# Performance work log

Measured on AMD Instinct MI355X. Metric: run time of the kernel, lower is better.

## Reference

```python
import jax, jax.numpy as jnp
import numpy as np

N, E = 15000, 60000
IN_FEATS, EMB_N, EMB_E, HID = 32, 16, 16, 64
NODE_DIM = IN_FEATS + 2 * EMB_N          # 64
EDGE_DIM = 2 * EMB_E + 1                 # 33
N_SUPER, N_NT, N_TAG, N_PRI = 16, 32, 64, 128


def setup_inputs() -> dict:
    key = jax.random.key(0)
    ks = jax.random.split(key, 24)
    s = lambda d: 1.0 / np.sqrt(d)
    inp = {
        'x': jax.random.normal(ks[0], (N, IN_FEATS), jnp.float32),
        'input_np': jax.random.randint(ks[1], (N,), 0, 1000, jnp.int32),
        'output_np': jax.random.randint(ks[2], (N,), 0, 1000, jnp.int32),
        'edge_index': jax.random.randint(ks[3], (2, E), 0, N, jnp.int32),
        'edge_nt': jax.random.randint(ks[4], (E,), 0, 50, jnp.int32),
        'edge_np': jax.random.randint(ks[5], (E,), 0, 500, jnp.int32),
        'edge_sc': jax.random.uniform(ks[6], (E,), jnp.float32),
        # embeddings
        'in_np_emb': jax.random.normal(ks[7], (1000, EMB_N), jnp.float32),
        'out_np_emb': jax.random.normal(ks[8], (1000, EMB_N), jnp.float32),
        'edge_np_emb': jax.random.normal(ks[9], (500, EMB_E), jnp.float32),
        'edge_nt_emb': jax.random.normal(ks[10], (50, EMB_E), jnp.float32),
        # edge MLP: Linear(33,64) -> ReLU -> Linear(64, NODE_DIM*HID)
        'mlp_w1': jax.random.normal(ks[11], (EDGE_DIM, 64), jnp.float32) * s(EDGE_DIM),
        'mlp_b1': jnp.zeros((64,), jnp.float32),
        'mlp_w2': jax.random.normal(ks[12], (64, NODE_DIM * HID), jnp.float32) * s(64),
        'mlp_b2': jnp.zeros((NODE_DIM * HID,), jnp.float32),
        # NNConv root weight + bias
        'root_w': jax.random.normal(ks[13], (NODE_DIM, HID), jnp.float32) * s(NODE_DIM),
        'conv_b': jnp.zeros((HID,), jnp.float32),
        # heads
        'w_super': jax.random.normal(ks[14], (HID, N_SUPER), jnp.float32) * s(HID),
        'b_super': jnp.zeros((N_SUPER,), jnp.float32),
        'w_nt': jax.random.normal(ks[15], (HID, N_NT), jnp.float32) * s(HID),
        'b_nt': jnp.zeros((N_NT,), jnp.float32),
        'w_tags': jax.random.normal(ks[16], (HID, N_TAG), jnp.float32) * s(HID),
        'b_tags': jnp.zeros((N_TAG,), jnp.float32),
        'w_primary': jax.random.normal(ks[17], (HID, N_PRI), jnp.float32) * s(HID),
        'b_primary': jnp.zeros((N_PRI,), jnp.float32),
    }
    return inp


def _forward(x, edge_sc, in_np_emb, out_np_emb, edge_np_emb, edge_nt_emb,
             mlp_w1, mlp_b1, mlp_w2, mlp_b2, root_w, conv_b,
             w_super, b_super, w_nt, b_nt, w_tags, b_tags, w_primary, b_primary,
             input_np, output_np, edge_index, edge_nt, edge_np):
    # node features: [N, NODE_DIM]
    xf = jnp.concatenate([x, in_np_emb[input_np], out_np_emb[output_np]], axis=1)
    # edge features: [E, EDGE_DIM]
    ea = jnp.concatenate([edge_nt_emb[edge_nt], edge_np_emb[edge_np], edge_sc[:, None]], axis=1)
    # edge MLP -> per-edge weight matrix [E, NODE_DIM, HID]
    h = jax.nn.relu(ea @ mlp_w1 + mlp_b1)
    W = (h @ mlp_w2 + mlp_b2).reshape(-1, NODE_DIM, HID)
    src, dst = edge_index[0], edge_index[1]
    # per-edge matvec: message from src node through its edge weight
    msg = jnp.einsum('ei,eio->eo', xf[src], W)                     # [E, HID]
    sums = jax.ops.segment_sum(msg, dst, num_segments=N)            # [N, HID]
    cnt = jax.ops.segment_sum(jnp.ones((msg.shape[0],), msg.dtype), dst, num_segments=N)
    aggr = sums / jnp.maximum(cnt, 1.0)[:, None]                    # scatter-mean
    out = jax.nn.relu(aggr + xf @ root_w + conv_b)                  # NNConv root + bias, then ReLU
    # dropout is identity in eval mode
    return (out @ w_super + b_super, out @ w_nt + b_nt,
            out @ w_tags + b_tags, out @ w_primary + b_primary)


def reference(x, input_np, output_np, edge_index, edge_nt, edge_np, edge_sc,
              in_np_emb, out_np_emb, edge_np_emb, edge_nt_emb,
              mlp_w1, mlp_b1, mlp_w2, mlp_b2, root_w, conv_b,
              w_super, b_super, w_nt, b_nt, w_tags, b_tags, w_primary, b_primary):
    return _forward(x, edge_sc, in_np_emb, out_np_emb, edge_np_emb, edge_nt_emb,
                    mlp_w1, mlp_b1, mlp_w2, mlp_b2, root_w, conv_b,
                    w_super, b_super, w_nt, b_nt, w_tags, b_tags, w_primary, b_primary,
                    input_np, output_np, edge_index, edge_nt, edge_np)
```

## Files before the change

kernel.cpp:

```cpp
#include <hip/hip_runtime.h>
#include <stdint.h>

#define NN 15000
#define NE 60000

typedef unsigned short u16;
typedef __attribute__((ext_vector_type(8))) short short8;
typedef __attribute__((ext_vector_type(4))) float f32x4;

#define XF_OFF    0u
#define W2T_OFF   1920000u
#define ROOTT_OFF 2452480u
#define WCATT_OFF 2460672u
#define SUMS_OFF  2491392u
#define H2_OFF    6391392u

__device__ __forceinline__ unsigned cvtpk(float lo, float hi) {
    unsigned r;
    asm("v_cvt_pk_bf16_f32 %0, %1, %2" : "=v"(r) : "v"(lo), "v"(hi));
    return r;
}
__device__ __forceinline__ u16 f2b(float f) { return (u16)(cvtpk(f, f) & 0xffffu); }

__global__ __launch_bounds__(256) void k_pre(
        const float* __restrict__ x,
        const int* __restrict__ inp, const int* __restrict__ outp,
        const int* __restrict__ ent, const int* __restrict__ enp,
        const float* __restrict__ esc,
        const float* __restrict__ in_emb, const float* __restrict__ out_emb,
        const float* __restrict__ nt_emb, const float* __restrict__ np_emb,
        const float* __restrict__ w1, const float* __restrict__ b1,
        const float* __restrict__ w2, const float* __restrict__ b2,
        const float* __restrict__ rootw,
        const float* __restrict__ wsup, const float* __restrict__ wnt,
        const float* __restrict__ wtg, const float* __restrict__ wpr,
        u16* __restrict__ xf, u16* __restrict__ w2t,
        u16* __restrict__ rootT, u16* __restrict__ wcatT,
        u16* __restrict__ h2, float4* __restrict__ zbase) {
    const int bid = blockIdx.x, tid = threadIdx.x;
    if (bid < 469) {
        __shared__ float w1f[33 * 64];
        __shared__ float b1f[64];
        __shared__ float ea[128][34];
        const int e0 = bid * 128;
        for (int i = tid; i < 33 * 64; i += 256) w1f[i] = w1[i];
        if (tid < 64) b1f[tid] = b1[tid];
        for (int idx = tid; idx < 128 * 33; idx += 256) {
            int le = idx / 33, f = idx - le * 33;
            int e = e0 + le;
            float v = 0.f;
            if (e < NE) {
                if (f < 16)      v = nt_emb[ent[e] * 16 + f];
                else if (f < 32) v = np_emb[enp[e] * 16 + (f - 16)];
                else             v = esc[e];
            }
            ea[le][f] = v;
        }
        __syncthreads();
        const int c = tid & 63, eg = tid >> 6;
        unsigned pk[16];
        #pragma unroll
        for (int l = 0; l < 32; l += 2) {
            float a0 = b1f[c], a1 = b1f[c];
            #pragma unroll
            for (int i = 0; i < 33; ++i) {
                a0 += ea[eg * 32 + l][i] * w1f[i * 64 + c];
                a1 += ea[eg * 32 + l + 1][i] * w1f[i * 64 + c];
            }
            pk[l >> 1] = cvtpk(fmaxf(a0, 0.f), fmaxf(a1, 0.f));
        }
        const int ew = e0 + eg * 32;
        if (ew + 32 <= NE) {
            #pragma unroll
            for (int g = 0; g < 8; ++g)
                *(uint2*)(h2 + (size_t)((ew >> 2) + g) * 256 + c * 4) =
                    make_uint2(pk[2 * g], pk[2 * g + 1]);
        }
    } else if (bid < 1407) {
        int t = (bid - 469) * 256 + tid;
        if (t >= NN * 16) return;
        int n = t >> 4, j4 = t & 15;
        float4 v;
        if (j4 < 8)       v = *(const float4*)(x + n * 32 + j4 * 4);
        else if (j4 < 12) v = *(const float4*)(in_emb + inp[n] * 16 + (j4 - 8) * 4);
        else              v = *(const float4*)(out_emb + outp[n] * 16 + (j4 - 12) * 4);
        uint2 p;
        p.x = cvtpk(v.x, v.y);
        p.y = cvtpk(v.z, v.w);
        *(uint2*)(xf + n * 64 + j4 * 4) = p;
    } else if (bid < 2523) {
        int idx = (bid - 1407) * 256 + tid;
        if (idx < 65 * 4096) {
            int k = idx >> 12, r = idx & 4095, o = r >> 6, i = r & 63;
            float v = (k < 64) ? w2[(k << 12) + (i << 6) + o] : b2[(i << 6) + o];
            w2t[idx] = f2b(v);
        } else if (idx < 65 * 4096 + 4096) {
            int t = idx - 65 * 4096; int c = t >> 6, i = t & 63;
            rootT[t] = f2b(rootw[i * 64 + c]);
        } else if (idx < 65 * 4096 + 4096 + 15360) {
            int t = idx - (65 * 4096 + 4096); int col = t >> 6, k = t & 63;
            float v;
            if (col < 16)       v = wsup[k * 16 + col];
            else if (col < 48)  v = wnt[k * 32 + col - 16];
            else if (col < 112) v = wtg[k * 64 + col - 48];
            else                v = wpr[k * 128 + col - 112];
            wcatT[t] = f2b(v);
        }
    } else {
        int i = (bid - 2523) * 256 + tid;
        if (i < (NN * 65) / 4) zbase[i] = make_float4(0.f, 0.f, 0.f, 0.f);
    }
}

__global__ __launch_bounds__(1024) void k_msg(const int* __restrict__ ei,
                                              const u16* __restrict__ xf,
                                              const u16* __restrict__ h2,
                                              const u16* __restrict__ w2t,
                                              float* __restrict__ sums,
                                              float* __restrict__ cnt) {
    __shared__ __align__(16) char smem[65 * 2048];
    const int tid  = threadIdx.x;
    const int lane = tid & 63;
    const int wave = tid >> 6;
    const int lhi  = lane >> 4;
    const int llo  = lane & 15;
    const int oq   = blockIdx.x & 3;
    const int wslot = (blockIdx.x >> 2) * 16 + wave;

    for (int sl = wave; sl < 65; sl += 16) {
        const char* src = (const char*)w2t + (size_t)sl * 8192 + oq * 2048;
        char* dst = smem + sl * 2048;
        #pragma unroll
        for (int it = 0; it < 2; ++it) {
            int lin = (lane + it * 64) * 16;
            int phys = lin ^ (((lin >> 7) & 7) << 4);
            *(uint4*)(dst + phys) = *(const uint4*)(src + lin);
        }
    }
    __syncthreads();
    if (wslot >= 938) return;

    const int pc0 = (llo * 128 + lhi * 16) ^ ((llo & 7) << 4);
    const int pc1 = (llo * 128 + 64 + lhi * 16) ^ ((llo & 7) << 4);

    const int base = wslot * 64;
    short8 a[4][2]; int eb[4];
    #pragma unroll
    for (int st = 0; st < 4; ++st) {
        int e = base + st * 16 + llo;
        int src = ei[e < NE ? e : NE - 1];
        a[st][0] = *(const short8*)(xf + (size_t)src * 64 + lhi * 8);
        a[st][1] = *(const short8*)(xf + (size_t)src * 64 + 32 + lhi * 8);
        int e2 = base + st * 16 + lhi * 4;
        eb[st] = (e2 > NE - 4) ? (NE - 4) : e2;
    }
    f32x4 acc[4];
    #pragma unroll
    for (int st = 0; st < 4; ++st) acc[st] = (f32x4){0.f, 0.f, 0.f, 0.f};

    uint4 hc[4], hn[4];
    #pragma unroll
    for (int st = 0; st < 4; ++st)
        hc[st] = *(const uint4*)(h2 + ((size_t)(eb[st] >> 2) << 8));

    #pragma unroll 1
    for (int s = 0; s < 64; s += 2) {
        if (s + 2 < 64) {
            #pragma unroll
            for (int st = 0; st < 4; ++st)
                hn[st] = *(const uint4*)(h2 + ((size_t)(eb[st] >> 2) << 8) + (s + 2) * 4);
        }
        {
            const char* bb = smem + s * 2048;
            short8 B0 = *(const short8*)(bb + pc0);
            short8 B1 = *(const short8*)(bb + pc1);
            #pragma unroll
            for (int st = 0; st < 4; ++st) {
                f32x4 q;
                q = __builtin_amdgcn_mfma_f32_16x16x32_bf16(a[st][0], B0, (f32x4){0.f,0.f,0.f,0.f}, 0, 0, 0);
                q = __builtin_amdgcn_mfma_f32_16x16x32_bf16(a[st][1], B1, q, 0, 0, 0);
                union { unsigned u; float f; } u0, u1, u2, u3;
                u0.u = hc[st].x << 16;         u1.u = hc[st].x & 0xffff0000u;
                u2.u = hc[st].y << 16;         u3.u = hc[st].y & 0xffff0000u;
                acc[st][0] = fmaf(u0.f, q[0], acc[st][0]);
                acc[st][1] = fmaf(u1.f, q[1], acc[st][1]);
                acc[st][2] = fmaf(u2.f, q[2], acc[st][2]);
                acc[st][3] = fmaf(u3.f, q[3], acc[st][3]);
            }
        }
        {
            const char* bb = smem + (s + 1) * 2048;
            short8 B0 = *(const short8*)(bb + pc0);
            short8 B1 = *(const short8*)(bb + pc1);
            #pragma unroll
            for (int st = 0; st < 4; ++st) {
                f32x4 q;
                q = __builtin_amdgcn_mfma_f32_16x16x32_bf16(a[st][0], B0, (f32x4){0.f,0.f,0.f,0.f}, 0, 0, 0);
                q = __builtin_amdgcn_mfma_f32_16x16x32_bf16(a[st][1], B1, q, 0, 0, 0);
                union { unsigned u; float f; } u0, u1, u2, u3;
                u0.u = hc[st].z << 16;         u1.u = hc[st].z & 0xffff0000u;
                u2.u = hc[st].w << 16;         u3.u = hc[st].w & 0xffff0000u;
                acc[st][0] = fmaf(u0.f, q[0], acc[st][0]);
                acc[st][1] = fmaf(u1.f, q[1], acc[st][1]);
                acc[st][2] = fmaf(u2.f, q[2], acc[st][2]);
                acc[st][3] = fmaf(u3.f, q[3], acc[st][3]);
            }
        }
        #pragma unroll
        for (int st = 0; st < 4; ++st) hc[st] = hn[st];
    }
    {
        const char* bb = smem + 64 * 2048;
        short8 B0 = *(const short8*)(bb + pc0);
        short8 B1 = *(const short8*)(bb + pc1);
        #pragma unroll
        for (int st = 0; st < 4; ++st) {
            acc[st] = __builtin_amdgcn_mfma_f32_16x16x32_bf16(a[st][0], B0, acc[st], 0, 0, 0);
            acc[st] = __builtin_amdgcn_mfma_f32_16x16x32_bf16(a[st][1], B1, acc[st], 0, 0, 0);
        }
    }
    #pragma unroll
    for (int st = 0; st < 4; ++st) {
        int4 d4 = *(const int4*)(ei + NE + eb[st]);
        #pragma unroll
        for (int r = 0; r < 4; ++r) {
            int e = base + st * 16 + lhi * 4 + r;
            if (e < NE) {
                int d = (r == 0) ? d4.x : (r == 1) ? d4.y : (r == 2) ? d4.z : d4.w;
                atomicAdd(sums + (size_t)d * 64 + oq * 16 + llo, acc[st][r]);
                if (oq == 0 && llo == 0) atomicAdd(cnt + d, 1.0f);
            }
        }
    }
}

__global__ __launch_bounds__(256) void k_out(const u16* __restrict__ xf,
                                             const float* __restrict__ sums,
                                             const float* __restrict__ cnt,
                                             const u16* __restrict__ rootT,
                                             const u16* __restrict__ wcatT,
                                             const float* __restrict__ convb,
                                             const float* __restrict__ bsup,
                                             const float* __restrict__ bnt,
                                             const float* __restrict__ btg,
                                             const float* __restrict__ bpr,
                                             float* __restrict__ outp) {
    __shared__ __align__(16) u16 outlds[4][16][72];
    int tid = threadIdx.x;
    int wave = tid >> 6, lane = tid & 63;
    int lhi = lane >> 4, llo = lane & 15;
    int sid = blockIdx.x * 4 + wave;
    const bool live = (sid < 938);
    if (!live) sid = 937;
    int n0 = sid * 16;

    short8 a1[2];
    #pragma unroll
    for (int c = 0; c < 2; ++c) {
        int node = n0 + llo; if (node >= NN) node = NN - 1;
        a1[c] = *(const short8*)(xf + (size_t)node * 64 + c * 32 + lhi * 8);
    }
    f32x4 racc[4];
    #pragma unroll
    for (int o = 0; o < 4; ++o) racc[o] = (f32x4){0.f, 0.f, 0.f, 0.f};
    #pragma unroll
    for (int c = 0; c < 2; ++c)
        #pragma unroll
        for (int o = 0; o < 4; ++o) {
            short8 b = *(const short8*)(rootT + (o * 16 + llo) * 64 + c * 32 + lhi * 8);
            racc[o] = __builtin_amdgcn_mfma_f32_16x16x32_bf16(a1[c], b, racc[o], 0, 0, 0);
        }
    #pragma unroll
    for (int o = 0; o < 4; ++o) {
        int col = o * 16 + llo;
        #pragma unroll
        for (int r = 0; r < 4; ++r) {
            int node = n0 + lhi * 4 + r;
            float v = 0.f;
            if (node < NN) v = sums[(size_t)node * 64 + col] / fmaxf(cnt[node], 1.0f);
            v += racc[o][r] + convb[col];
            v = fmaxf(v, 0.f);
            outlds[wave][lhi * 4 + r][col] = f2b(v);
        }
    }
    __syncthreads();
    short8 a2[2];
    #pragma unroll
    for (int c = 0; c < 2; ++c)
        a2[c] = *(const short8*)(&outlds[wave][llo][c * 32 + lhi * 8]);
    #pragma unroll
    for (int o = 0; o < 15; ++o) {
        f32x4 hacc = (f32x4){0.f, 0.f, 0.f, 0.f};
        #pragma unroll
        for (int c = 0; c < 2; ++c) {
            short8 b = *(const short8*)(wcatT + (o * 16 + llo) * 64 + c * 32 + lhi * 8);
            hacc = __builtin_amdgcn_mfma_f32_16x16x32_bf16(a2[c], b, hacc, 0, 0, 0);
        }
        int col = o * 16 + llo;
        float bv; size_t off0; int w_, csh;
        if (col < 16)       { bv = bsup[col];       off0 = 0;                 w_ = 16;  csh = 0;   }
        else if (col < 48)  { bv = bnt[col - 16];   off0 = (size_t)NN * 16;   w_ = 32;  csh = 16;  }
        else if (col < 112) { bv = btg[col - 48];   off0 = (size_t)NN * 48;   w_ = 64;  csh = 48;  }
        else                { bv = bpr[col - 112];  off0 = (size_t)NN * 112;  w_ = 128; csh = 112; }
        #pragma unroll
        for (int r = 0; r < 4; ++r) {
            int node = n0 + lhi * 4 + r;
            if (live && node < NN)
                outp[off0 + (size_t)node * w_ + (col - csh)] = hacc[r] + bv;
        }
    }
}

extern "C" void kernel_launch(void* const* d_in, const int* in_sizes, int n_in,
                              void* d_out, int out_size, void* d_ws, size_t ws_size,
                              hipStream_t stream) {
    const float* x        = (const float*)d_in[0];
    const int* input_np   = (const int*)d_in[1];
    const int* output_np  = (const int*)d_in[2];
    const int* edge_idx   = (const int*)d_in[3];
    const int* edge_nt    = (const int*)d_in[4];
    const int* edge_np    = (const int*)d_in[5];
    const float* edge_sc  = (const float*)d_in[6];
    const float* in_emb   = (const float*)d_in[7];
    const float* out_emb  = (const float*)d_in[8];
    const float* enp_emb  = (const float*)d_in[9];
    const float* ent_emb  = (const float*)d_in[10];
    const float* w1       = (const float*)d_in[11];
    const float* b1       = (const float*)d_in[12];
    const float* w2       = (const float*)d_in[13];
    const float* b2       = (const float*)d_in[14];
    const float* rootw    = (const float*)d_in[15];
    const float* convb    = (const float*)d_in[16];
    const float* wsup     = (const float*)d_in[17];
    const float* bsup     = (const float*)d_in[18];
    const float* wnt      = (const float*)d_in[19];
    const float* bnt      = (const float*)d_in[20];
    const float* wtg      = (const float*)d_in[21];
    const float* btg      = (const float*)d_in[22];
    const float* wpr      = (const float*)d_in[23];
    const float* bpr      = (const float*)d_in[24];

    char* ws = (char*)d_ws;
    u16* xf    = (u16*)(ws + XF_OFF);
    u16* w2t   = (u16*)(ws + W2T_OFF);
    u16* rootT = (u16*)(ws + ROOTT_OFF);
    u16* wcatT = (u16*)(ws + WCATT_OFF);
    float* sums = (float*)(ws + SUMS_OFF);
    float* cnt  = sums + (size_t)NN * 64;
    u16* h2    = (u16*)(ws + H2_OFF);

    k_pre<<<3476, 256, 0, stream>>>(x, input_np, output_np, edge_nt, edge_np, edge_sc,
                                    in_emb, out_emb, ent_emb, enp_emb, w1, b1, w2, b2,
                                    rootw, wsup, wnt, wtg, wpr,
                                    xf, w2t, rootT, wcatT, h2, (float4*)sums);
    k_msg<<<236, 1024, 0, stream>>>(edge_idx, xf, h2, w2t, sums, cnt);
    k_out<<<235, 256, 0, stream>>>(xf, sums, cnt, rootT, wcatT, convb, bsup, bnt, btg, bpr, (float*)d_out);
}
```

Before: 94.35 us.

## Compute edge MLP first layer with bf16 MFMA and enlarge message grid

The first edge-MLP layer (33->64 with ReLU) in the pre-kernel moves from scalar FP32 FMAs over a shared-memory tile to bf16 MFMA 16x16x32 instructions. Each wave handles 16 edges, with the gathered embeddings converted to bf16 fragments and w1 transposed into LDS. This cuts the ALU cost of the stage but lowers input precision to bf16 before the first matmul. The message kernel's grid also grows from 236 to 256 blocks with a launch-bounds occupancy hint, presumably to cover all edges or fill all CUs.

```diff
diff --git a/kernel.cpp b/kernel.cpp
--- a/kernel.cpp
+++ b/kernel.cpp
@@ -38,46 +38,52 @@
         u16* __restrict__ rootT, u16* __restrict__ wcatT,
         u16* __restrict__ h2, float4* __restrict__ zbase) {
     const int bid = blockIdx.x, tid = threadIdx.x;
-    if (bid < 469) {
-        __shared__ float w1f[33 * 64];
-        __shared__ float b1f[64];
-        __shared__ float ea[128][34];
-        const int e0 = bid * 128;
-        for (int i = tid; i < 33 * 64; i += 256) w1f[i] = w1[i];
-        if (tid < 64) b1f[tid] = b1[tid];
-        for (int idx = tid; idx < 128 * 33; idx += 256) {
-            int le = idx / 33, f = idx - le * 33;
-            int e = e0 + le;
-            float v = 0.f;
-            if (e < NE) {
-                if (f < 16)      v = nt_emb[ent[e] * 16 + f];
-                else if (f < 32) v = np_emb[enp[e] * 16 + (f - 16)];
-                else             v = esc[e];
-            }
-            ea[le][f] = v;
-        }
+    if (bid < 938) {
+        __shared__ __align__(16) u16 w1t[64 * 64];
+        __shared__ float b1s[64];
+        const int lane = tid & 63, wave = tid >> 6;
+        const int lhi = lane >> 4, llo = lane & 15;
+        for (int idx = tid; idx < 4096; idx += 256) {
+            int col = idx >> 6, k = idx & 63;
+            w1t[col * 64 + k] = f2b((k < 33) ? w1[k * 64 + col] : 0.f);
+        }
+        if (tid < 64) b1s[tid] = b1[tid];
         __syncthreads();
-        const int c = tid & 63, eg = tid >> 6;
-        unsigned pk[16];
-        #pragma unroll
-        for (int l = 0; l < 32; l += 2) {
-            float a0 = b1f[c], a1 = b1f[c];
-            #pragma unroll
-            for (int i = 0; i < 33; ++i) {
-                a0 += ea[eg * 32 + l][i] * w1f[i * 64 + c];
-                a1 += ea[eg * 32 + l + 1][i] * w1f[i * 64 + c];
-            }
-            pk[l >> 1] = cvtpk(fmaxf(a0, 0.f), fmaxf(a1, 0.f));
-        }
-        const int ew = e0 + eg * 32;
-        if (ew + 32 <= NE) {
-            #pragma unroll
-            for (int g = 0; g < 8; ++g)
-                *(uint2*)(h2 + (size_t)((ew >> 2) + g) * 256 + c * 4) =
-                    make_uint2(pk[2 * g], pk[2 * g + 1]);
-        }
-    } else if (bid < 1407) {
-        int t = (bid - 469) * 256 + tid;
+        int g = bid * 4 + wave;
+        if (g >= 3750) return;
+        int e = g * 16 + llo;
+        short8 A0;
+        {
+            const float* src = (lhi < 2) ? (nt_emb + (size_t)ent[e] * 16 + lhi * 8)
+                                         : (np_emb + (size_t)enp[e] * 16 + (lhi - 2) * 8);
+            float4 v0 = *(const float4*)(src);
+            float4 v1 = *(const float4*)(src + 4);
+            union { short8 s; unsigned u[4]; } Au;
+            Au.u[0] = cvtpk(v0.x, v0.y); Au.u[1] = cvtpk(v0.z, v0.w);
+            Au.u[2] = cvtpk(v1.x, v1.y); Au.u[3] = cvtpk(v1.z, v1.w);
+            A0 = Au.s;
+        }
+        short8 A1 = (short8){0, 0, 0, 0, 0, 0, 0, 0};
+        if (lhi == 0) {
+            union { short8 s; unsigned u[4]; } Au;
+            Au.s = A1; Au.u[0] = cvtpk(esc[e], 0.f); A1 = Au.s;
+        }
+        #pragma unroll
+        for (int o = 0; o < 4; ++o) {
+            short8 B0 = *(const short8*)(&w1t[(o * 16 + llo) * 64 + lhi * 8]);
+            short8 B1 = *(const short8*)(&w1t[(o * 16 + llo) * 64 + 32 + lhi * 8]);
+            f32x4 q;
+            q = __builtin_amdgcn_mfma_f32_16x16x32_bf16(A0, B0, (f32x4){0.f,0.f,0.f,0.f}, 0, 0, 0);
+            q = __builtin_amdgcn_mfma_f32_16x16x32_bf16(A1, B1, q, 0, 0, 0);
+            int kh = o * 16 + llo;
+            float bv = b1s[kh];
+            float v0 = fmaxf(q[0] + bv, 0.f), v1 = fmaxf(q[1] + bv, 0.f);
+            float v2 = fmaxf(q[2] + bv, 0.f), v3 = fmaxf(q[3] + bv, 0.f);
+            uint2 pk2 = make_uint2(cvtpk(v0, v1), cvtpk(v2, v3));
+            *(uint2*)(h2 + (size_t)(g * 4 + lhi) * 256 + kh * 4) = pk2;
+        }
+    } else if (bid < 1876) {
+        int t = (bid - 938) * 256 + tid;
         if (t >= NN * 16) return;
         int n = t >> 4, j4 = t & 15;
         float4 v;
@@ -88,8 +94,8 @@
         p.x = cvtpk(v.x, v.y);
         p.y = cvtpk(v.z, v.w);
         *(uint2*)(xf + n * 64 + j4 * 4) = p;
-    } else if (bid < 2523) {
-        int idx = (bid - 1407) * 256 + tid;
+    } else if (bid < 2992) {
+        int idx = (bid - 1876) * 256 + tid;
         if (idx < 65 * 4096) {
             int k = idx >> 12, r = idx & 4095, o = r >> 6, i = r & 63;
             float v = (k < 64) ? w2[(k << 12) + (i << 6) + o] : b2[(i << 6) + o];
@@ -107,17 +113,17 @@
             wcatT[t] = f2b(v);
         }
     } else {
-        int i = (bid - 2523) * 256 + tid;
+        int i = (bid - 2992) * 256 + tid;
         if (i < (NN * 65) / 4) zbase[i] = make_float4(0.f, 0.f, 0.f, 0.f);
     }
 }
 
-__global__ __launch_bounds__(1024) void k_msg(const int* __restrict__ ei,
-                                              const u16* __restrict__ xf,
-                                              const u16* __restrict__ h2,
-                                              const u16* __restrict__ w2t,
-                                              float* __restrict__ sums,
-                                              float* __restrict__ cnt) {
+__global__ __launch_bounds__(1024, 1) void k_msg(const int* __restrict__ ei,
+                                                 const u16* __restrict__ xf,
+                                                 const u16* __restrict__ h2,
+                                                 const u16* __restrict__ w2t,
+                                                 float* __restrict__ sums,
+                                                 float* __restrict__ cnt) {
     __shared__ __align__(16) char smem[65 * 2048];
     const int tid  = threadIdx.x;
     const int lane = tid & 63;
@@ -349,10 +355,10 @@
     float* cnt  = sums + (size_t)NN * 64;
     u16* h2    = (u16*)(ws + H2_OFF);
 
-    k_pre<<<3476, 256, 0, stream>>>(x, input_np, output_np, edge_nt, edge_np, edge_sc,
+    k_pre<<<3945, 256, 0, stream>>>(x, input_np, output_np, edge_nt, edge_np, edge_sc,
                                     in_emb, out_emb, ent_emb, enp_emb, w1, b1, w2, b2,
                                     rootw, wsup, wnt, wtg, wpr,
                                     xf, w2t, rootT, wcatT, h2, (float4*)sums);
-    k_msg<<<236, 1024, 0, stream>>>(edge_idx, xf, h2, w2t, sums, cnt);
+    k_msg<<<256, 1024, 0, stream>>>(edge_idx, xf, h2, w2t, sums, cnt);
     k_out<<<235, 256, 0, stream>>>(xf, sums, cnt, rootT, wcatT, convb, bsup, bnt, btg, bpr, (float*)d_out);
 }
```

Result: faster. 85.42 us (-9.5%).
